# Kernel optimization log

Hardware: AMD Instinct MI355X
Metric: run time of the kernel (lower is better)

The kernel has to match this reference:

```python
import jax, jax.numpy as jnp
import numpy as np

B, N, DIM = 2, 2048, 1024
HEADS, DIM_HEAD = 8, 64
INNER = HEADS * DIM_HEAD  # 512
EPS = 1e-5  # fp32 branch of the source LayerNorm


def setup_inputs() -> dict:
    key = jax.random.key(0)
    ks = jax.random.split(key, 5)
    x = jax.random.normal(ks[0], (B, N, DIM), dtype=jnp.float32)
    g = jnp.ones((DIM,), dtype=jnp.float32)  # LayerNorm gain init
    # Linear weights stored as (in, out) so y = x @ W. Source zero-inits
    # to_out; we use small random values so the baseline output is nonzero.
    wq = jax.random.normal(ks[1], (DIM, INNER), dtype=jnp.float32) * 0.02
    wkv = jax.random.normal(ks[2], (DIM, 2 * INNER), dtype=jnp.float32) * 0.02
    wo = jax.random.normal(ks[3], (INNER, DIM), dtype=jnp.float32) * 0.02
    return {"x": x, "g": g, "wq": wq, "wkv": wkv, "wo": wo}


def reference(x, g, wq, wkv, wo):
    # Custom LayerNorm from the source: statistics over dim=1 (sequence axis!)
    mean = jnp.mean(x, axis=1, keepdims=True)
    var = jnp.var(x, axis=1, keepdims=True)  # unbiased=False
    xn = (x - mean) * jax.lax.rsqrt(var + EPS) * g  # g broadcasts on last dim

    q = xn @ wq                      # [b, n, inner]
    kv = xn @ wkv                    # [b, n, 2*inner]
    k, v = jnp.split(kv, 2, axis=-1)

    def split_heads(t):  # b n (h d) -> b h n d
        b, n, _ = t.shape
        return t.reshape(b, n, HEADS, DIM_HEAD).transpose(0, 2, 1, 3)

    q, k, v = map(split_heads, (q, k, v))
    q = q * (DIM_HEAD ** -0.5)

    sim = jnp.einsum('bhid,bhjd->bhij', q, k)   # [b, h, n, n]
    attn = jax.nn.softmax(sim, axis=-1)
    out = jnp.einsum('bhij,bhjd->bhid', attn, v)  # [b, h, n, d]

    out = out.transpose(0, 2, 1, 3).reshape(B, N, INNER)  # b h n d -> b n (h d)
    return out @ wo  # [b, n, dim]
```

## Files before the change

kernel.cpp:

```cpp
#include <hip/hip_runtime.h>
#include <hip/hip_bf16.h>
#include <stdint.h>


#define B_ 2
#define N_ 2048
#define DIM_ 1024
#define DH_ 64
#define INNER_ 512
#define ROWS_ 4096
#define BHSTRIDE 131072

#define QSCALE 0.18033688011112042f

typedef __bf16 bf16x8 __attribute__((ext_vector_type(8)));
typedef float floatx4 __attribute__((ext_vector_type(4)));

#if __has_builtin(__builtin_amdgcn_exp2f)
#define EXP2(x) __builtin_amdgcn_exp2f(x)
#else
#define EXP2(x) exp2f(x)
#endif

__device__ __forceinline__ ushort f2bf(float f) {
    union { __bf16 h; ushort u; } v;
    v.h = (__bf16)f;
    return v.u;
}
#if __has_builtin(__builtin_amdgcn_cvt_pk_bf16_f32)
__device__ __forceinline__ uint32_t pkbf(float a, float b) {
    auto h = __builtin_amdgcn_cvt_pk_bf16_f32(a, b);
    union { decltype(h) h; uint32_t u; } v;
    v.h = h;
    return v.u;
}
#else
__device__ __forceinline__ uint32_t pkbf(float a, float b) {
    return (uint32_t)f2bf(a) | ((uint32_t)f2bf(b) << 16);
}
#endif

__device__ __forceinline__ size_t frag_off(int m, int k, int nkc) {
    return ((size_t)((m >> 4) * nkc + (k >> 5)) * 64 +
            (size_t)((m & 15) | (((k >> 3) & 3) << 4))) * 8 + (k & 7);
}

__global__ __launch_bounds__(256) void setup_fused(
    const float* __restrict__ x, float* __restrict__ ps, float* __restrict__ pq,
    const float* __restrict__ wq, const float* __restrict__ wkv,
    const float* __restrict__ wo, ushort* __restrict__ wqkv_f,
    ushort* __restrict__ wo_f) {
    __shared__ float tile[32][33];
    int bid = blockIdx.x;
    if (bid < 256) {
        int gd = (bid & 7) * 256 + threadIdx.x;
        int ch = bid >> 3;
        int b = gd >> 10;
        const float* p = x + (size_t)(b * N_ + ch * 64) * DIM_ + (gd & 1023);
        float s = 0.f, q = 0.f;
#pragma unroll 16
        for (int n = 0; n < 64; ++n) { float v = p[(size_t)n * DIM_]; s += v; q += v * v; }
        ps[ch * 2048 + gd] = s;
        pq[ch * 2048 + gd] = q;
        return;
    }
    int t = bid - 256;
    const float* src; ushort* dst; int C, K, k0, ncol0, nglob0; float scale;
    if (t < 512) {
        int kt = t >> 4, nt = t & 15;
        src = wq; dst = wqkv_f; C = 512; K = 1024; scale = QSCALE;
        k0 = kt * 32; ncol0 = nt * 32; nglob0 = ncol0;
    } else if (t < 1536) {
        int u = t - 512; int kt = u >> 5, nt = u & 31;
        src = wkv; dst = wqkv_f; C = 1024; K = 1024; scale = 1.f;
        k0 = kt * 32; ncol0 = nt * 32; nglob0 = 512 + ncol0;
    } else {
        int u = t - 1536; int kt = u >> 5, nt = u & 31;
        src = wo; dst = wo_f; C = 1024; K = 512; scale = 1.f;
        k0 = kt * 32; ncol0 = nt * 32; nglob0 = ncol0;
    }
    int ti = threadIdx.x >> 5, tj = threadIdx.x & 31;
#pragma unroll
    for (int p = 0; p < 4; ++p)
        tile[ti + 8 * p][tj] = src[(size_t)(k0 + ti + 8 * p) * C + ncol0 + tj] * scale;
    __syncthreads();
    if (threadIdx.x < 128) {
        int nl = threadIdx.x & 31, kc8 = threadIdx.x >> 5;
        union { ushort us[8]; uint4 v; } u;
#pragma unroll
        for (int ii = 0; ii < 8; ++ii) u.us[ii] = f2bf(tile[kc8 * 8 + ii][nl]);
        *(uint4*)&dst[frag_off(nglob0 + nl, k0 + kc8 * 8, K >> 5)] = u.v;
    }
}

__global__ __launch_bounds__(256) void finalize_norm(
    const float* __restrict__ ps, const float* __restrict__ pq,
    const float* __restrict__ x, const float* __restrict__ g,
    ushort* __restrict__ xnf) {
    __shared__ float s4[4][64], q4[4][64], aa[64], bb[64];
    int t = threadIdx.x;
    int b = blockIdx.x >> 8, slab = (blockIdx.x >> 4) & 15, nch = blockIdx.x & 15;
    int c0 = slab * 64;
    {
        int c = t & 63, grp = t >> 6;
        float s = 0.f, q = 0.f;
#pragma unroll
        for (int ch = 0; ch < 8; ++ch) {
            int o = (grp * 8 + ch) * 2048 + b * 1024 + c0 + c;
            s += ps[o]; q += pq[o];
        }
        s4[grp][c] = s; q4[grp][c] = q;
    }
    __syncthreads();
    if (t < 64) {
        float s = s4[0][t] + s4[1][t] + s4[2][t] + s4[3][t];
        float q = q4[0][t] + q4[1][t] + q4[2][t] + q4[3][t];
        float mean = s * (1.f / N_);
        float var = q * (1.f / N_) - mean * mean;
        float rstd = rsqrtf(var + 1e-5f);
        float a = rstd * g[c0 + t];
        aa[t] = a; bb[t] = -mean * a;
    }
    __syncthreads();
    int c4 = (t & 15) * 4, ro = t >> 4;
#pragma unroll
    for (int it = 0; it < 8; ++it) {
        int r = nch * 128 + it * 16 + ro;
        int m = b * 2048 + r;
        float4 xv = *(const float4*)&x[(size_t)m * DIM_ + c0 + c4];
        float v0 = xv.x * aa[c4 + 0] + bb[c4 + 0];
        float v1 = xv.y * aa[c4 + 1] + bb[c4 + 1];
        float v2 = xv.z * aa[c4 + 2] + bb[c4 + 2];
        float v3 = xv.w * aa[c4 + 3] + bb[c4 + 3];
        uint2 u; u.x = pkbf(v0, v1); u.y = pkbf(v2, v3);
        *(uint2*)&xnf[frag_off(m, c0 + c4, 32)] = u;
    }
}

template <int NKC>
__device__ __forceinline__ void gemm_core(
    const ushort* __restrict__ pA, const ushort* __restrict__ pB,
    floatx4 (&acc)[4][4]) {
    constexpr int TS = NKC * 512;
    bf16x8 a0[4], b0[4], a1[4], b1[4], a2[4], b2[4];
    auto ld = [&](bf16x8 (&a)[4], bf16x8 (&b)[4], int kc) {
#pragma unroll
        for (int i = 0; i < 4; ++i) {
            a[i] = *(const bf16x8*)(pA + (size_t)i * TS + (size_t)kc * 512);
            b[i] = *(const bf16x8*)(pB + (size_t)i * TS + (size_t)kc * 512);
        }
    };
    auto mm = [&](bf16x8 (&a)[4], bf16x8 (&b)[4]) {
#pragma unroll
        for (int mi = 0; mi < 4; ++mi)
#pragma unroll
            for (int ni = 0; ni < 4; ++ni)
                acc[mi][ni] = __builtin_amdgcn_mfma_f32_16x16x32_bf16(
                    a[mi], b[ni], acc[mi][ni], 0, 0, 0);
    };
    ld(a0, b0, 0);
    ld(a1, b1, 1);
    int kc = 0;
    for (; kc + 3 <= NKC; kc += 3) {
        ld(a2, b2, kc + 2);
        mm(a0, b0);
        if (kc + 3 < NKC) ld(a0, b0, kc + 3);
        mm(a1, b1);
        if (kc + 4 < NKC) ld(a1, b1, kc + 4);
        mm(a2, b2);
    }
    if (NKC % 3 >= 1) mm(a0, b0);
    if (NKC % 3 == 2) mm(a1, b1);
}

__global__ __launch_bounds__(256) void gemm_qkv(
    const ushort* __restrict__ xnf, const ushort* __restrict__ wf,
    ushort* __restrict__ qf, ushort* __restrict__ kf, ushort* __restrict__ vf) {
    int tx = threadIdx.x, w = tx >> 6, l = tx & 63;
    int wr = w >> 1, wc = w & 1;
    int lr = l & 15, lq = l >> 4;
    int bid = blockIdx.x;
    int xcd = bid & 7, t = bid >> 3;
    int bx = xcd * 4 + (t & 3);
    int by = t >> 2;
    int rx = bx * 2 + wr;
    const ushort* pA = xnf + (size_t)(rx * 4) * 32 * 512 + l * 8;
    const ushort* pB = wf + (size_t)(by * 8 + wc * 4) * 32 * 512 + l * 8;
    floatx4 acc[4][4] = {};
    gemm_core<32>(pA, pB, acc);
    int col0 = by * 128 + wc * 64;
    int bb2 = (rx * 64) >> 11;
    if (by < 8) {
        ushort* qkbase = (by < 4) ? qf : kf;
#pragma unroll
        for (int ni = 0; ni < 4; ++ni) {
            int col = col0 + 16 * ni + lr;
            int hh = (col >> 6) & 7, d = col & 63;
            ushort* base = qkbase + (size_t)(bb2 * 8 + hh) * BHSTRIDE
                           + (d >> 5) * 512 + ((d >> 3) & 3) * 128 + (d & 7)
                           + (4 * lq) * 8;
#pragma unroll
            for (int mi = 0; mi < 4; ++mi) {
                size_t o2 = (size_t)((rx * 4 + mi) & 127) * 1024;
#pragma unroll
                for (int reg = 0; reg < 4; ++reg)
                    base[o2 + reg * 8] = f2bf(acc[mi][ni][reg]);
            }
        }
    } else {
#pragma unroll
        for (int ni = 0; ni < 4; ++ni) {
            int cv = col0 - 1024 + 16 * ni + lr;
            int hh = cv >> 6, d = cv & 63;
            ushort* base = vf + (size_t)(bb2 * 8 + hh) * BHSTRIDE
                           + (d >> 4) * 32768 + (d & 15) * 8;
#pragma unroll
            for (int mi = 0; mi < 4; ++mi) {
                int nn = (rx * 64 + 16 * mi + 4 * lq) & 2047;
                uint2 u;
                u.x = pkbf(acc[mi][ni][0], acc[mi][ni][1]);
                u.y = pkbf(acc[mi][ni][2], acc[mi][ni][3]);
                *(uint2*)&base[(nn >> 5) * 512 + ((nn >> 3) & 3) * 128 + (nn & 7)] = u;
            }
        }
    }
}

__global__ __launch_bounds__(256) void gemm_out(
    const ushort* __restrict__ af, const ushort* __restrict__ wf,
    float* __restrict__ out) {
    int tx = threadIdx.x, w = tx >> 6, l = tx & 63;
    int wr = w >> 1, wc = w & 1;
    int lr = l & 15, lq = l >> 4;
    int bid = blockIdx.x;
    int xcd = bid & 7, t = bid >> 3;
    int bx = xcd * 4 + (t & 3);
    int by = t >> 2;
    int rx = bx * 2 + wr;
    const ushort* pA = af + (size_t)(rx * 4) * 16 * 512 + l * 8;
    const ushort* pB = wf + (size_t)(by * 8 + wc * 4) * 16 * 512 + l * 8;
    floatx4 acc[4][4] = {};
    gemm_core<16>(pA, pB, acc);
    int col0 = by * 128 + wc * 64;
#pragma unroll
    for (int mi = 0; mi < 4; ++mi)
#pragma unroll
        for (int ni = 0; ni < 4; ++ni) {
            int col = col0 + 16 * ni + lr;
#pragma unroll
            for (int reg = 0; reg < 4; ++reg) {
                int row = rx * 64 + 16 * mi + 4 * lq + reg;
                out[(size_t)row * 1024 + col] = acc[mi][ni][reg];
            }
        }
}

__global__ __launch_bounds__(512, 2) void flash_attn(
    const ushort* __restrict__ qf, const ushort* __restrict__ kf,
    const ushort* __restrict__ vf, ushort* __restrict__ attnf) {
    __shared__ __align__(16) float sArena[8 * 4352];
    __shared__ float sL[8][64];

    const int tx = threadIdx.x;
    const int w = tx >> 6, l = tx & 63;
    const int qsel = w >> 2, kq = w & 3;
    const int lr = l & 15, lq = l >> 4;
    const int bid = blockIdx.x;
    const int bh = (bid & 7) * 2 + ((bid >> 3) & 1);
    const int qt = bid >> 4;

    const ushort* qfb = qf + (size_t)bh * BHSTRIDE
                        + (size_t)(qt * 8 + qsel * 4) * 1024 + l * 8;
    const ushort* kfb = kf + (size_t)bh * BHSTRIDE + (size_t)kq * 32768 + l * 8;
    const ushort* vfb = vf + (size_t)bh * BHSTRIDE + (size_t)kq * 8192 + l * 8;
    ushort* sPw = (ushort*)(sArena + w * 4352);

    bf16x8 bq[4][2];
#pragma unroll
    for (int qq = 0; qq < 4; ++qq)
#pragma unroll
        for (int s = 0; s < 2; ++s)
            bq[qq][s] = *(const bf16x8*)(qfb + qq * 1024 + s * 512);

    floatx4 o[4][4] = {};
    float lsum[4] = {0.f, 0.f, 0.f, 0.f};

    bf16x8 ak[8], bv[8];
#pragma unroll
    for (int kk = 0; kk < 4; ++kk) {
        ak[kk * 2 + 0] = *(const bf16x8*)(kfb + kk * 1024);
        ak[kk * 2 + 1] = *(const bf16x8*)(kfb + kk * 1024 + 512);
    }

    for (int kt = 0; kt < 8; ++kt) {
#pragma unroll
        for (int dt = 0; dt < 4; ++dt) {
            bv[dt * 2 + 0] = *(const bf16x8*)(vfb + dt * 32768 + (kt * 2 + 0) * 512);
            bv[dt * 2 + 1] = *(const bf16x8*)(vfb + dt * 32768 + (kt * 2 + 1) * 512);
        }

#pragma unroll
        for (int h = 0; h < 2; ++h) {
            floatx4 c[2][4] = {};
            __builtin_amdgcn_s_setprio(1);
#pragma unroll
            for (int s = 0; s < 2; ++s)
#pragma unroll
                for (int kk = 0; kk < 2; ++kk)
#pragma unroll
                    for (int qq = 0; qq < 4; ++qq)
                        c[kk][qq] = __builtin_amdgcn_mfma_f32_16x16x32_bf16(
                            ak[(2 * h + kk) * 2 + s], bq[qq][s], c[kk][qq], 0, 0, 0);
            __builtin_amdgcn_s_setprio(0);

            if (h == 1 && kt + 1 < 8) {
                const ushort* kp = kfb + (size_t)(kt + 1) * 4096;
#pragma unroll
                for (int kk = 0; kk < 4; ++kk) {
                    ak[kk * 2 + 0] = *(const bf16x8*)(kp + kk * 1024);
                    ak[kk * 2 + 1] = *(const bf16x8*)(kp + kk * 1024 + 512);
                }
            }

#pragma unroll
            for (int kk = 0; kk < 2; ++kk)
#pragma unroll
                for (int qq = 0; qq < 4; ++qq) {
                    float e0 = EXP2(c[kk][qq][0]);
                    float e1 = EXP2(c[kk][qq][1]);
                    float e2 = EXP2(c[kk][qq][2]);
                    float e3 = EXP2(c[kk][qq][3]);
                    lsum[qq] += (e0 + e1) + (e2 + e3);
                    uint2 u; u.x = pkbf(e0, e1); u.y = pkbf(e2, e3);
                    *(uint2*)&sPw[(16 * qq + lr) * 72 + 16 * (2 * h + kk) + 4 * lq] = u;
                }
        }

#pragma unroll
        for (int s = 0; s < 2; ++s) {
            bf16x8 ap[4];
#pragma unroll
            for (int mi = 0; mi < 4; ++mi)
                ap[mi] = *(const bf16x8*)&sPw[(16 * mi + lr) * 72 + 32 * s + 8 * lq];
            __builtin_amdgcn_s_setprio(1);
#pragma unroll
            for (int mi = 0; mi < 4; ++mi)
#pragma unroll
                for (int dt = 0; dt < 4; ++dt)
                    o[mi][dt] = __builtin_amdgcn_mfma_f32_16x16x32_bf16(
                        ap[mi], bv[dt * 2 + s], o[mi][dt], 0, 0, 0);
            __builtin_amdgcn_s_setprio(0);
        }
    }

#pragma unroll
    for (int qq = 0; qq < 4; ++qq) {
        lsum[qq] += __shfl_xor(lsum[qq], 16);
        lsum[qq] += __shfl_xor(lsum[qq], 32);
    }

    float* Rw = sArena + w * 4352;
#pragma unroll
    for (int mi = 0; mi < 4; ++mi)
#pragma unroll
        for (int dt = 0; dt < 4; ++dt)
#pragma unroll
            for (int reg = 0; reg < 4; ++reg)
                Rw[(16 * mi + 4 * lq + reg) * 68 + 16 * dt + lr] = o[mi][dt][reg];
    if (lq == 0) {
#pragma unroll
        for (int qq = 0; qq < 4; ++qq) sL[w][16 * qq + lr] = lsum[qq];
    }
    __syncthreads();

    const int g = qsel;
    int qloc = 16 * (w & 3) + (l >> 2);
    int c0 = (l & 3) * 16;
    float4 acc[4];
#pragma unroll
    for (int rg = 0; rg < 4; ++rg) {
        const float* R = sArena + (g * 4 + rg) * 4352 + qloc * 68 + c0;
#pragma unroll
        for (int c = 0; c < 4; ++c) {
            float4 v = *(const float4*)&R[4 * c];
            if (rg == 0) acc[c] = v;
            else { acc[c].x += v.x; acc[c].y += v.y; acc[c].z += v.z; acc[c].w += v.w; }
        }
    }
    float ltot = sL[g * 4 + 0][qloc] + sL[g * 4 + 1][qloc]
               + sL[g * 4 + 2][qloc] + sL[g * 4 + 3][qloc];
    float inv = 1.f / ltot;
    int m = (bh >> 3) * 2048 + qt * 128 + g * 64 + qloc;
    int kb = (bh & 7) * 64 + c0;
#pragma unroll
    for (int c = 0; c < 4; ++c) {
        uint2 u;
        u.x = pkbf(acc[c].x * inv, acc[c].y * inv);
        u.y = pkbf(acc[c].z * inv, acc[c].w * inv);
        *(uint2*)&attnf[frag_off(m, kb + 4 * c, 16)] = u;
    }
}

extern "C" void kernel_launch(void* const* d_in, const int* in_sizes, int n_in,
                              void* d_out, int out_size, void* d_ws, size_t ws_size,
                              hipStream_t stream) {
    const float* x   = (const float*)d_in[0];
    const float* g   = (const float*)d_in[1];
    const float* wq  = (const float*)d_in[2];
    const float* wkv = (const float*)d_in[3];
    const float* wo  = (const float*)d_in[4];
    float* out = (float*)d_out;

    char* ws = (char*)d_ws;
    float*  psum   = (float*)(ws + 0);
    float*  psqr   = (float*)(ws + 262144);
    ushort* xnf    = (ushort*)(ws + 524288);
    ushort* wqkv_f = (ushort*)(ws + 8912896);
    ushort* wo_f   = (ushort*)(ws + 12058624);
    ushort* qfb    = (ushort*)(ws + 13107200);
    ushort* kfb    = (ushort*)(ws + 17301504);
    ushort* vfb    = (ushort*)(ws + 21495808);
    ushort* attnf  = (ushort*)(ws + 25690112);

    setup_fused<<<2304, 256, 0, stream>>>(x, psum, psqr, wq, wkv, wo, wqkv_f, wo_f);
    finalize_norm<<<512, 256, 0, stream>>>(psum, psqr, x, g, xnf);
    gemm_qkv<<<384, 256, 0, stream>>>(xnf, wqkv_f, qfb, kfb, vfb);
    flash_attn<<<256, 512, 0, stream>>>(qfb, kfb, vfb, attnf);
    gemm_out<<<256, 256, 0, stream>>>(attnf, wo_f, out);
}
```

Measured before the change: 140.4 us.

## Stage QKV GEMM operand tiles through double-buffered LDS with direct global-to-LDS loads

The QKV projection GEMM no longer has each wave load its own A/B fragments straight from global memory. Each block now cooperatively stages its 8 A chunks and 8 B chunks per k-step into a double-buffered shared-memory tile, using global_load_lds when available. The waves then read their fragments from LDS, so operands shared between the two waves of a row or column are fetched from global memory once. This cuts redundant global traffic but adds a __syncthreads per k-step and LDS read latency in place of the previous triple-buffered register prefetch.

```diff
diff --git a/kernel.cpp b/kernel.cpp
--- a/kernel.cpp
+++ b/kernel.cpp
@@ -37,6 +37,19 @@
 #else
 __device__ __forceinline__ uint32_t pkbf(float a, float b) {
     return (uint32_t)f2bf(a) | ((uint32_t)f2bf(b) << 16);
+}
+#endif
+
+#if __has_builtin(__builtin_amdgcn_global_load_lds)
+__device__ __forceinline__ void gld_lds16(const ushort* g, ushort* s) {
+    __builtin_amdgcn_global_load_lds(
+        (const __attribute__((address_space(1))) unsigned int*)g,
+        (__attribute__((address_space(3))) unsigned int*)s, 16, 0, 0);
+}
+#else
+__device__ __forceinline__ void gld_lds16(const ushort* g, ushort* s) {
+    int l = threadIdx.x & 63;
+    *(uint4*)(s + l * 8) = *(const uint4*)g;
 }
 #endif
 
@@ -176,6 +189,7 @@
 __global__ __launch_bounds__(256) void gemm_qkv(
     const ushort* __restrict__ xnf, const ushort* __restrict__ wf,
     ushort* __restrict__ qf, ushort* __restrict__ kf, ushort* __restrict__ vf) {
+    __shared__ __align__(16) ushort sAB[2][16][512];
     int tx = threadIdx.x, w = tx >> 6, l = tx & 63;
     int wr = w >> 1, wc = w & 1;
     int lr = l & 15, lq = l >> 4;
@@ -184,10 +198,43 @@
     int bx = xcd * 4 + (t & 3);
     int by = t >> 2;
     int rx = bx * 2 + wr;
-    const ushort* pA = xnf + (size_t)(rx * 4) * 32 * 512 + l * 8;
-    const ushort* pB = wf + (size_t)(by * 8 + wc * 4) * 32 * 512 + l * 8;
+
+    const ushort* gsrc[4];
+#pragma unroll
+    for (int c = 0; c < 4; ++c) {
+        int ch = w * 4 + c;
+        gsrc[c] = (ch < 8)
+            ? xnf + (size_t)(bx * 8 + ch) * (32 * 512) + l * 8
+            : wf  + (size_t)(by * 8 + (ch - 8)) * (32 * 512) + l * 8;
+    }
+    auto stage = [&](int buf, int kc) {
+#pragma unroll
+        for (int c = 0; c < 4; ++c)
+            gld_lds16(gsrc[c] + (size_t)kc * 512, &sAB[buf][w * 4 + c][0]);
+    };
+
     floatx4 acc[4][4] = {};
-    gemm_core<32>(pA, pB, acc);
+    stage(0, 0);
+    __syncthreads();
+    int cur = 0;
+    for (int kc = 0; kc < 32; ++kc) {
+        if (kc + 1 < 32) stage(cur ^ 1, kc + 1);
+        bf16x8 a[4], b[4];
+#pragma unroll
+        for (int i = 0; i < 4; ++i) {
+            a[i] = *(const bf16x8*)&sAB[cur][wr * 4 + i][l * 8];
+            b[i] = *(const bf16x8*)&sAB[cur][8 + wc * 4 + i][l * 8];
+        }
+#pragma unroll
+        for (int mi = 0; mi < 4; ++mi)
+#pragma unroll
+            for (int ni = 0; ni < 4; ++ni)
+                acc[mi][ni] = __builtin_amdgcn_mfma_f32_16x16x32_bf16(
+                    a[mi], b[ni], acc[mi][ni], 0, 0, 0);
+        __syncthreads();
+        cur ^= 1;
+    }
+
     int col0 = by * 128 + wc * 64;
     int bb2 = (rx * 64) >> 11;
     if (by < 8) {
```

Result: no change. 142.8 us (+1.7%).
